# Kernel optimization log

Measured on AMD Instinct MI355X. Metric: run time of the kernel, lower is better.

## Reference

```python
import jax, jax.numpy as jnp
from jax import lax
import numpy as np

P = 9  # patch_size


def unfold9(img):
    # img: (C, H, W) -> (C, P*P, L) with L = (H//P)*(W//P), non-overlapping patches
    C, H, W = img.shape
    x = img.reshape(C, H // P, P, W // P, P)
    x = x.transpose(0, 2, 4, 1, 3).reshape(C, P * P, (H // P) * (W // P))
    return x


def fold9(blocks, H, W):
    # blocks: (C, P*P, L) -> (C, H, W), inverse of unfold9 (no overlaps)
    C = blocks.shape[0]
    x = blocks.reshape(C, P, P, H // P, W // P)
    return x.transpose(0, 3, 1, 4, 2).reshape(C, H, W)


def avgpool3d_k3s2p1(x):
    # AvgPool3d(kernel=3, stride=2, padding=1, count_include_pad=False) on (B,C,D,H,W)
    win = (1, 1, 3, 3, 3)
    strides = (1, 1, 2, 2, 2)
    pad = [(0, 0), (0, 0), (1, 1), (1, 1), (1, 1)]
    s = lax.reduce_window(x, 0.0, lax.add, win, strides, pad)
    cnt = lax.reduce_window(jnp.ones_like(x[:1, :1]), 0.0, lax.add, win, strides, pad)
    return s / cnt


def setup_inputs() -> dict:
    key = jax.random.key(0)
    k = jax.random.split(key, 7)
    in1, in2, out = 32, 64, 64
    x = jax.random.normal(k[0], (1, in1, 36, 72, 72), jnp.float32)
    y = jax.random.normal(k[1], (1, in2, 18, 36, 36), jnp.float32)
    z = jax.random.normal(k[2], (1, out, 36, 72, 72), jnp.float32)
    w_img = jax.random.normal(k[3], (out, in1), jnp.float32) * 0.05
    b_img = jax.random.normal(k[4], (out,), jnp.float32) * 0.01
    w_fea = jax.random.normal(k[5], (out, in2), jnp.float32) * 0.05
    b_fea = jax.random.normal(k[6], (out,), jnp.float32) * 0.01
    return {"x": x, "y": y, "z": z, "w_img": w_img, "b_img": b_img,
            "w_fea": w_fea, "b_fea": b_fea}


def reference(x, y, z, w_img, b_img, w_fea, b_fea):
    # 1x1x1 conv projections (pointwise channel mix)
    xq = jnp.einsum('bcdhw,oc->bodhw', x, w_img) + b_img[None, :, None, None, None]
    yk = jnp.einsum('bcdhw,oc->bodhw', y, w_fea) + b_fea[None, :, None, None, None]
    C = xq.shape[1]
    D1, HW1 = xq.shape[2], xq.shape[3] * xq.shape[4]
    D2, HW2 = yk.shape[2], yk.shape[3] * yk.shape[4]
    Ux = unfold9(xq.reshape(C, D1, HW1))          # (C, 81, L1)
    Uy = unfold9(yk.reshape(C, D2, HW2))          # (C, 81, L2)
    att = jnp.einsum('ckl,ckm->clm', Ux, Uy)      # (C, L1, L2) per-channel patch attn

    # --- Cross_head ---
    Dd, Hd, Wd = z.shape[2], z.shape[3], z.shape[4]
    dec = z.reshape(C, Dd, Hd * Wd)               # decoder_reshape
    xd = avgpool3d_k3s2p1(z)                      # (1, C, Dd', Hd', Wd')
    Dp, HWp = xd.shape[2], xd.shape[3] * xd.shape[4]
    Uxd = unfold9(xd.reshape(C, Dp, HWp))         # (C, 81, L2)
    # count_nonzero along L2 (non-differentiable, matches torch)
    nz = jnp.sum(att != 0, axis=-1).astype(att.dtype) + 1e-5  # (C, L1)
    corr_blocks = jnp.einsum('clm,ckm->ckl', att / nz[:, :, None], Uxd)  # (C, 81, L1)
    corr = fold9(corr_blocks, Dd, Hd * Wd)        # (C, Dd, Hd*Wd)
    act = jnp.where(corr > 0, corr, 0.2 * corr)   # LeakyReLU(0.2)
    out = act * dec + dec
    return out.reshape(z.shape)
```

## Files before the change

kernel.cpp:

```cpp
#include <hip/hip_runtime.h>
#include <hip/hip_bf16.h>

typedef __hip_bfloat16 bf16;
typedef float in_t;
typedef float out_t;
typedef __attribute__((ext_vector_type(8))) short short8;
typedef __attribute__((ext_vector_type(4))) float f32x4;

#define CH    64
#define CIN1  32
#define CIN2  64
#define S1    186624
#define W1    5184
#define S2    23328
#define W2    1296
#define BSTR  104
#define ASTR  104
#define OSTR  136
#define YSTR  68
#define HWSTR 76
#define INV_NZ (1.0f/(288.0f + 1e-5f))

#define NB_PL 2304
#define NB_PX 1458
#define NB_PY 365
#define NBT   (NB_PL + NB_PX + NB_PY)
#define NBR   (NBT - NB_PL)

static __device__ __forceinline__ unsigned short f2bu(float f) {
    bf16 h = __float2bfloat16(f);
    unsigned short u;
    __builtin_memcpy(&u, &h, 2);
    return u;
}

__global__ __launch_bounds__(256) void k_stage1(
    const in_t* __restrict__ x, const in_t* __restrict__ wi, const in_t* __restrict__ bi,
    bf16* __restrict__ xq,
    const in_t* __restrict__ y, const in_t* __restrict__ wf, const in_t* __restrict__ bf,
    unsigned short* __restrict__ yk,
    const in_t* __restrict__ z, unsigned short* __restrict__ xd)
{
    __shared__ __align__(16) char smem[17408];
    int t = threadIdx.x;
    long long i = blockIdx.x;

    long long pb = (i*NB_PL)/NBT;
    bool is_pool = ((i+1)*NB_PL)/NBT > pb;
    long long r  = i - pb;
    long long yb = (r*NB_PY)/NBR;
    bool is_py   = !is_pool && (((r+1)*NB_PY)/NBR > yb);

    if (is_pool) {
        int bid = (int)pb;
        float* dsum = reinterpret_cast<float*>(smem);
        int c  = bid / 36;
        int rr = bid - c*36;
        int od = rr >> 1, half = rr & 1;
        int hbase = half ? 35 : 0;
        int nrows = half ? 37 : 36;
        int oh0   = half ? 18 : 0;
        int dlo = od ? 2*od - 1 : 0;
        int nd  = od ? 3 : 2;
        const float* zb = z + ((size_t)c*36 + dlo)*W1;
        for (int ii = t; ii < nrows*18; ii += 256) {
            int rw = ii / 18, q = ii - (ii/18)*18;
            int off = (hbase + rw)*18 + q;
            const float4* p0 = reinterpret_cast<const float4*>(zb);
            float4 a = p0[off], b = p0[1296 + off];
            float4 s;
            if (nd == 3) {
                float4 e = p0[2592 + off];
                s = (float4){ a.x+b.x+e.x, a.y+b.y+e.y, a.z+b.z+e.z, a.w+b.w+e.w };
            } else {
                s = (float4){ a.x+b.x, a.y+b.y, a.z+b.z, a.w+b.w };
            }
            *reinterpret_cast<float4*>(&dsum[rw*HWSTR + q*4]) = s;
        }
        __syncthreads();
        float icd = (nd == 3) ? (1.f/3.f) : 0.5f;
        unsigned short* xdp = xd + (size_t)c*S2 + (size_t)od*W2 + oh0*36;
        for (int idx = t; idx < 648; idx += 256) {
            int ohl = idx / 36, ow = idx - (idx/36)*36;
            int oh = oh0 + ohl;
            int h0 = oh ? 2*oh-1 : 0, h1 = 2*oh+1;
            int w0 = ow ? 2*ow-1 : 0, w1 = 2*ow+1;
            float s = 0.f;
            for (int h = h0; h <= h1; ++h) {
                int lr = h - hbase;
                for (int w = w0; w <= w1; ++w)
                    s += dsum[lr*HWSTR + w];
            }
            float ich = (h1 - h0) == 1 ? 0.5f : (1.f/3.f);
            float icw = (w1 - w0) == 1 ? 0.5f : (1.f/3.f);
            xdp[idx] = f2bu(s * icd * ich * icw);
        }
    } else if (!is_py) {
        int gs0 = (int)(r - yb)*128;
        int l = t & 63, wv = t >> 6;
        int lcol = l & 15, loct = l >> 4;

        ushort4 rr4[2][4];
        #pragma unroll
        for (int mt = 0; mt < 2; ++mt) {
            int scol = gs0 + (wv*2 + mt)*16 + lcol;
            union { short8 v; unsigned short u[8]; } af;
            #pragma unroll
            for (int j = 0; j < 8; ++j)
                af.u[j] = f2bu(x[(size_t)(loct*8 + j)*S1 + scol]);
            #pragma unroll
            for (int og = 0; og < 4; ++og) {
                int o = og*16 + lcol;
                union { short8 v; unsigned short u[8]; } wfr;
                float4 a  = *reinterpret_cast<const float4*>(&wi[o*CIN1 + loct*8]);
                float4 bq = *reinterpret_cast<const float4*>(&wi[o*CIN1 + loct*8 + 4]);
                wfr.u[0]=f2bu(a.x);  wfr.u[1]=f2bu(a.y);
                wfr.u[2]=f2bu(a.z);  wfr.u[3]=f2bu(a.w);
                wfr.u[4]=f2bu(bq.x); wfr.u[5]=f2bu(bq.y);
                wfr.u[6]=f2bu(bq.z); wfr.u[7]=f2bu(bq.w);
                float bo = bi[o];
                f32x4 d = { bo, bo, bo, bo };
                d = __builtin_amdgcn_mfma_f32_16x16x32_bf16(af.v, wfr.v, d, 0, 0, 0);
                rr4[mt][og] = (ushort4){ f2bu(d[0]), f2bu(d[1]), f2bu(d[2]), f2bu(d[3]) };
            }
        }
        unsigned short* ot = reinterpret_cast<unsigned short*>(smem);
        #pragma unroll
        for (int mt = 0; mt < 2; ++mt)
            #pragma unroll
            for (int og = 0; og < 4; ++og)
                *reinterpret_cast<ushort4*>(
                    &ot[(og*16 + lcol)*OSTR + wv*32 + mt*16 + loct*4]) = rr4[mt][og];
        __syncthreads();
        #pragma unroll
        for (int j = 0; j < 4; ++j) {
            int row = wv*16 + j*4 + (l >> 4);
            int c8  = l & 15;
            uint4 v = *reinterpret_cast<const uint4*>(&ot[row*OSTR + c8*8]);
            *reinterpret_cast<uint4*>(
                (unsigned short*)xq + (size_t)row*S1 + gs0 + c8*8) = v;
        }
    } else {
        int pyb   = (int)yb;
        int sblk0 = pyb*64;
        int wv = t >> 6, l = t & 63;
        int lcol = l & 15, loct = l >> 4;
        int tile = pyb*4 + wv;
        unsigned short* ot = reinterpret_cast<unsigned short*>(smem);
        if (tile < 1458) {
            int s0 = tile*16;
            union { short8 v; unsigned short u[8]; } af[2];
            #pragma unroll
            for (int kk = 0; kk < 2; ++kk)
                #pragma unroll
                for (int j = 0; j < 8; ++j)
                    af[kk].u[j] = f2bu(y[(size_t)(kk*32 + loct*8 + j)*S2 + s0 + lcol]);
            #pragma unroll
            for (int og = 0; og < 4; ++og) {
                int o = og*16 + lcol;
                union { short8 v; unsigned short u[8]; } wfr[2];
                #pragma unroll
                for (int kk = 0; kk < 2; ++kk) {
                    float4 a  = *reinterpret_cast<const float4*>(&wf[o*CIN2 + kk*32 + loct*8]);
                    float4 bq = *reinterpret_cast<const float4*>(&wf[o*CIN2 + kk*32 + loct*8 + 4]);
                    wfr[kk].u[0]=f2bu(a.x);  wfr[kk].u[1]=f2bu(a.y);
                    wfr[kk].u[2]=f2bu(a.z);  wfr[kk].u[3]=f2bu(a.w);
                    wfr[kk].u[4]=f2bu(bq.x); wfr[kk].u[5]=f2bu(bq.y);
                    wfr[kk].u[6]=f2bu(bq.z); wfr[kk].u[7]=f2bu(bq.w);
                }
                float bo = bf[o];
                f32x4 d = { bo, bo, bo, bo };
                d = __builtin_amdgcn_mfma_f32_16x16x32_bf16(af[0].v, wfr[0].v, d, 0, 0, 0);
                d = __builtin_amdgcn_mfma_f32_16x16x32_bf16(af[1].v, wfr[1].v, d, 0, 0, 0);
                ushort4 r4 = { f2bu(d[0]), f2bu(d[1]), f2bu(d[2]), f2bu(d[3]) };
                *reinterpret_cast<ushort4*>(&ot[(og*16 + lcol)*YSTR + wv*16 + loct*4]) = r4;
            }
        }
        __syncthreads();
        #pragma unroll
        for (int j = 0; j < 4; ++j) {
            int row = wv*16 + j*4 + (l >> 4);
            int c4  = l & 15;
            int s   = sblk0 + c4*4;
            if (s < S2) {
                ushort4 v = *reinterpret_cast<const ushort4*>(&ot[row*YSTR + c4*4]);
                *reinterpret_cast<ushort4*>(&yk[(size_t)row*S2 + s]) = v;
            }
        }
    }
}

__global__ __launch_bounds__(256) void k_M(
    const unsigned short* __restrict__ xd, const unsigned short* __restrict__ yk,
    unsigned short* __restrict__ Mg)
{
    __shared__ __align__(16) unsigned short Al[96*ASTR];
    __shared__ __align__(16) unsigned short Bl[96*ASTR];
    int c = blockIdx.x;
    int t = threadIdx.x;
    int l = t & 63, wv = t >> 6;
    int lcol = l & 15, lhi = l >> 4;
    int wr = wv >> 1, wc = wv & 1;

    for (int idx = t; idx < 15*ASTR; idx += 256) {
        Al[81*ASTR + idx] = 0;
        Bl[81*ASTR + idx] = 0;
    }

    f32x4 acc[3][3];
    #pragma unroll
    for (int a = 0; a < 3; ++a)
        #pragma unroll
        for (int b = 0; b < 3; ++b)
            acc[a][b] = (f32x4){0.f,0.f,0.f,0.f};

    const unsigned short* xc = xd + (size_t)c*S2;
    const unsigned short* yc = yk + (size_t)c*S2;

    for (int q = 0; q < 3; ++q) {
        __syncthreads();
        for (int idx = t; idx < 1944; idx += 256) {
            int r18 = idx / 108, u4 = idx - r18*108;
            int srcoff = r18*W2 + q*432 + u4*4;
            ushort4 va = *reinterpret_cast<const ushort4*>(xc + srcoff);
            ushort4 vb = *reinterpret_cast<const ushort4*>(yc + srcoff);
            int ph2 = r18 / 9, i2 = r18 - ph2*9;
            unsigned short ua[4] = {va.x, va.y, va.z, va.w};
            unsigned short ub[4] = {vb.x, vb.y, vb.z, vb.w};
            #pragma unroll
            for (int j = 0; j < 4; ++j) {
                int cc  = u4*4 + j;
                int pw2 = cc / 9, j2 = cc - pw2*9;
                int row = i2*9 + j2;
                int mp  = pw2*2 + ph2;
                Al[row*ASTR + mp] = ua[j];
                Bl[row*ASTR + mp] = ub[j];
            }
        }
        __syncthreads();
        #pragma unroll
        for (int kk = 0; kk < 3; ++kk) {
            short8 afr[3], bfr[3];
            #pragma unroll
            for (int a = 0; a < 3; ++a)
                afr[a] = *reinterpret_cast<const short8*>(
                    &Al[(wr*48 + a*16 + lcol)*ASTR + kk*32 + lhi*8]);
            #pragma unroll
            for (int b = 0; b < 3; ++b)
                bfr[b] = *reinterpret_cast<const short8*>(
                    &Bl[(wc*48 + b*16 + lcol)*ASTR + kk*32 + lhi*8]);
            #pragma unroll
            for (int a = 0; a < 3; ++a)
                #pragma unroll
                for (int b = 0; b < 3; ++b)
                    acc[a][b] = __builtin_amdgcn_mfma_f32_16x16x32_bf16(
                        afr[a], bfr[b], acc[a][b], 0, 0, 0);
        }
    }
    unsigned short* Mc = Mg + (size_t)c*9216;
    #pragma unroll
    for (int a = 0; a < 3; ++a)
        #pragma unroll
        for (int b = 0; b < 3; ++b)
            #pragma unroll
            for (int rr = 0; rr < 4; ++rr) {
                int k1 = wr*48 + a*16 + lhi*4 + rr;
                int k2 = wc*48 + b*16 + lcol;
                Mc[k1*96 + k2] = f2bu(acc[a][b][rr]);
            }
}

__global__ __launch_bounds__(256, 4) void k_corr(
    const unsigned short* __restrict__ Mg, const bf16* __restrict__ xq,
    const in_t* __restrict__ z, out_t* __restrict__ out)
{
    __shared__ __align__(16) unsigned short Pl[192*BSTR];
    int bid = blockIdx.x;
    int c   = bid / 12;
    int rem = bid - c*12;
    int ph  = rem / 3;
    int ck  = rem - ph*3;
    int colbase = ck*1728;
    int t = threadIdx.x;

    for (int idx = t; idx < 192*15; idx += 256) {
        int r = idx/15;
        Pl[r*BSTR + 81 + (idx - r*15)] = 0;
    }
    const unsigned short* xqu =
        (const unsigned short*)(xq + (size_t)c*S1 + (size_t)(ph*9)*W1 + colbase);
    for (int idx = t; idx < 3888; idx += 256) {
        int i2 = idx / 432, v4 = idx - i2*432;
        ushort4 vv = *reinterpret_cast<const ushort4*>(xqu + (size_t)i2*W1 + v4*4);
        int col = v4*4;
        unsigned short uu[4] = {vv.x, vv.y, vv.z, vv.w};
        #pragma unroll
        for (int j = 0; j < 4; ++j) {
            int cc = col + j;
            int p = cc/9, j2 = cc - p*9;
            Pl[p*BSTR + i2*9 + j2] = uu[j];
        }
    }
    __syncthreads();

    int wv = t >> 6, l = t & 63;
    int lrow = l & 15, lhi = l >> 4;

    short8 bfr[3][3];
    #pragma unroll
    for (int ntl = 0; ntl < 3; ++ntl) {
        int n = (wv*3 + ntl)*16 + lrow;
        #pragma unroll
        for (int kk = 0; kk < 3; ++kk)
            bfr[ntl][kk] = *reinterpret_cast<const short8*>(&Pl[n*BSTR + kk*32 + lhi*8]);
    }

    f32x4 acc[6][3];
    #pragma unroll
    for (int mt = 0; mt < 6; ++mt)
        #pragma unroll
        for (int ntl = 0; ntl < 3; ++ntl)
            acc[mt][ntl] = (f32x4){0.f,0.f,0.f,0.f};

    const unsigned short* Mc = Mg + c*9216;
    #pragma unroll
    for (int mt = 0; mt < 6; ++mt) {
        short8 afr[3];
        #pragma unroll
        for (int kk = 0; kk < 3; ++kk)
            afr[kk] = *reinterpret_cast<const short8*>(Mc + (mt*16 + lrow)*96 + kk*32 + lhi*8);
        #pragma unroll
        for (int ntl = 0; ntl < 3; ++ntl) {
            f32x4 d = acc[mt][ntl];
            #pragma unroll
            for (int kk = 0; kk < 3; ++kk)
                d = __builtin_amdgcn_mfma_f32_16x16x32_bf16(afr[kk], bfr[ntl][kk], d, 0, 0, 0);
            acc[mt][ntl] = d;
        }
    }
    __syncthreads();

    float* stage = reinterpret_cast<float*>(Pl);
    #pragma unroll
    for (int pass = 0; pass < 2; ++pass) {
        if ((wv >> 1) == pass) {
            #pragma unroll
            for (int mt = 0; mt < 6; ++mt)
                #pragma unroll
                for (int ntl = 0; ntl < 3; ++ntl) {
                    int n = (wv*3 + ntl)*16 + lrow - pass*96;
                    #pragma unroll
                    for (int r = 0; r < 4; ++r) {
                        int m = mt*16 + lhi*4 + r;
                        if (m <= 80) {
                            int i = m/9, j = m - 9*i;
                            stage[i*864 + n*9 + j] = acc[mt][ntl][r];
                        }
                    }
                }
        }
        __syncthreads();
        for (int idx = t; idx < 1944; idx += 256) {
            int i = idx/216, c4 = idx - i*216;
            float4 sv = *reinterpret_cast<const float4*>(&stage[i*864 + c4*4]);
            int ga = c*S1 + (ph*9 + i)*W1 + colbase + pass*864 + c4*4;
            float4 dv = *reinterpret_cast<const float4*>(&z[ga]);
            float4 ov;
            float cr;
            cr = sv.x*INV_NZ; ov.x = dv.x + (cr > 0.f ? cr : 0.2f*cr)*dv.x;
            cr = sv.y*INV_NZ; ov.y = dv.y + (cr > 0.f ? cr : 0.2f*cr)*dv.y;
            cr = sv.z*INV_NZ; ov.z = dv.z + (cr > 0.f ? cr : 0.2f*cr)*dv.z;
            cr = sv.w*INV_NZ; ov.w = dv.w + (cr > 0.f ? cr : 0.2f*cr)*dv.w;
            *reinterpret_cast<float4*>(&out[ga]) = ov;
        }
        __syncthreads();
    }
}

extern "C" void kernel_launch(void* const* d_in, const int* in_sizes, int n_in,
                              void* d_out, int out_size, void* d_ws, size_t ws_size,
                              hipStream_t stream)
{
    (void)in_sizes; (void)n_in; (void)out_size; (void)ws_size;
    const in_t* x     = (const in_t*)d_in[0];
    const in_t* y     = (const in_t*)d_in[1];
    const in_t* z     = (const in_t*)d_in[2];
    const in_t* w_img = (const in_t*)d_in[3];
    const in_t* b_img = (const in_t*)d_in[4];
    const in_t* w_fea = (const in_t*)d_in[5];
    const in_t* b_fea = (const in_t*)d_in[6];
    out_t* out = (out_t*)d_out;

    char* ws = (char*)d_ws;
    bf16*           xq = (bf16*)          (ws + 0);
    unsigned short* yk = (unsigned short*)(ws + 23887872);
    unsigned short* xd = (unsigned short*)(ws + 26873856);
    unsigned short* Mg = (unsigned short*)(ws + 29859840);

    hipLaunchKernelGGL(k_stage1, dim3(NBT), dim3(256), 0, stream,
                       x, w_img, b_img, xq, y, w_fea, b_fea, yk, z, xd);
    hipLaunchKernelGGL(k_M,      dim3(64),  dim3(256), 0, stream, xd, yk, Mg);
    hipLaunchKernelGGL(k_corr,   dim3(768), dim3(256), 0, stream, Mg, xq, z, out);
}
```

Measured before the change: 66.26 us.

## Fuse per-channel M computation into k_corr and drop the separate k_M launch

The k_M kernel is folded into k_corr. Each k_corr block now recomputes the 96x96 per-channel M matrix from xd and yk in shared memory and reads it from LDS, instead of reading it from a global buffer written by a separate 64-block launch. This removes one kernel launch, the global round trip for M, and a stage that ran on only 64 blocks. In exchange, M is recomputed 12 times per channel, which adds xd/yk loads and MFMA work to every block. The larger shared-memory footprint also lowers the occupancy bound from 4 to 2 blocks per CU.

```diff
diff --git a/kernel.cpp b/kernel.cpp
--- a/kernel.cpp
+++ b/kernel.cpp
@@ -15,7 +15,6 @@
 #define S2    23328
 #define W2    1296
 #define BSTR  104
-#define ASTR  104
 #define OSTR  136
 #define YSTR  68
 #define HWSTR 76
@@ -190,33 +189,39 @@
     }
 }
 
-__global__ __launch_bounds__(256) void k_M(
+__global__ __launch_bounds__(256, 2) void k_corr(
     const unsigned short* __restrict__ xd, const unsigned short* __restrict__ yk,
-    unsigned short* __restrict__ Mg)
+    const bf16* __restrict__ xq, const in_t* __restrict__ z, out_t* __restrict__ out)
 {
-    __shared__ __align__(16) unsigned short Al[96*ASTR];
-    __shared__ __align__(16) unsigned short Bl[96*ASTR];
-    int c = blockIdx.x;
+    __shared__ __align__(16) char smem[59904];
+    unsigned short* Al = reinterpret_cast<unsigned short*>(smem);
+    unsigned short* Bl = reinterpret_cast<unsigned short*>(smem) + 96*BSTR;
+    unsigned short* Ml = reinterpret_cast<unsigned short*>(smem) + 2*96*BSTR;
+    unsigned short* Pl = reinterpret_cast<unsigned short*>(smem);
+    int bid = blockIdx.x;
+    int c   = bid / 12;
+    int rem = bid - c*12;
+    int ph  = rem / 3;
+    int ck  = rem - ph*3;
+    int colbase = ck*1728;
     int t = threadIdx.x;
-    int l = t & 63, wv = t >> 6;
+    int wv = t >> 6, l = t & 63;
     int lcol = l & 15, lhi = l >> 4;
+
     int wr = wv >> 1, wc = wv & 1;
-
-    for (int idx = t; idx < 15*ASTR; idx += 256) {
-        Al[81*ASTR + idx] = 0;
-        Bl[81*ASTR + idx] = 0;
-    }
-
-    f32x4 acc[3][3];
+    for (int idx = t; idx < 15*BSTR; idx += 256) {
+        Al[81*BSTR + idx] = 0;
+        Bl[81*BSTR + idx] = 0;
+    }
+    f32x4 macc[3][3];
     #pragma unroll
     for (int a = 0; a < 3; ++a)
         #pragma unroll
         for (int b = 0; b < 3; ++b)
-            acc[a][b] = (f32x4){0.f,0.f,0.f,0.f};
+            macc[a][b] = (f32x4){0.f,0.f,0.f,0.f};
 
     const unsigned short* xc = xd + (size_t)c*S2;
     const unsigned short* yc = yk + (size_t)c*S2;
-
     for (int q = 0; q < 3; ++q) {
         __syncthreads();
         for (int idx = t; idx < 1944; idx += 256) {
@@ -233,8 +238,8 @@
                 int pw2 = cc / 9, j2 = cc - pw2*9;
                 int row = i2*9 + j2;
                 int mp  = pw2*2 + ph2;
-                Al[row*ASTR + mp] = ua[j];
-                Bl[row*ASTR + mp] = ub[j];
+                Al[row*BSTR + mp] = ua[j];
+                Bl[row*BSTR + mp] = ub[j];
             }
         }
         __syncthreads();
@@ -244,20 +249,19 @@
             #pragma unroll
             for (int a = 0; a < 3; ++a)
                 afr[a] = *reinterpret_cast<const short8*>(
-                    &Al[(wr*48 + a*16 + lcol)*ASTR + kk*32 + lhi*8]);
+                    &Al[(wr*48 + a*16 + lcol)*BSTR + kk*32 + lhi*8]);
             #pragma unroll
             for (int b = 0; b < 3; ++b)
                 bfr[b] = *reinterpret_cast<const short8*>(
-                    &Bl[(wc*48 + b*16 + lcol)*ASTR + kk*32 + lhi*8]);
+                    &Bl[(wc*48 + b*16 + lcol)*BSTR + kk*32 + lhi*8]);
             #pragma unroll
             for (int a = 0; a < 3; ++a)
                 #pragma unroll
                 for (int b = 0; b < 3; ++b)
-                    acc[a][b] = __builtin_amdgcn_mfma_f32_16x16x32_bf16(
-                        afr[a], bfr[b], acc[a][b], 0, 0, 0);
-        }
-    }
-    unsigned short* Mc = Mg + (size_t)c*9216;
+                    macc[a][b] = __builtin_amdgcn_mfma_f32_16x16x32_bf16(
+                        afr[a], bfr[b], macc[a][b], 0, 0, 0);
+        }
+    }
     #pragma unroll
     for (int a = 0; a < 3; ++a)
         #pragma unroll
@@ -266,22 +270,9 @@
             for (int rr = 0; rr < 4; ++rr) {
                 int k1 = wr*48 + a*16 + lhi*4 + rr;
                 int k2 = wc*48 + b*16 + lcol;
-                Mc[k1*96 + k2] = f2bu(acc[a][b][rr]);
-            }
-}
-
-__global__ __launch_bounds__(256, 4) void k_corr(
-    const unsigned short* __restrict__ Mg, const bf16* __restrict__ xq,
-    const in_t* __restrict__ z, out_t* __restrict__ out)
-{
-    __shared__ __align__(16) unsigned short Pl[192*BSTR];
-    int bid = blockIdx.x;
-    int c   = bid / 12;
-    int rem = bid - c*12;
-    int ph  = rem / 3;
-    int ck  = rem - ph*3;
-    int colbase = ck*1728;
-    int t = threadIdx.x;
+                Ml[k1*BSTR + k2] = f2bu(macc[a][b][rr]);
+            }
+    __syncthreads();
 
     for (int idx = t; idx < 192*15; idx += 256) {
         int r = idx/15;
@@ -303,8 +294,7 @@
     }
     __syncthreads();
 
-    int wv = t >> 6, l = t & 63;
-    int lrow = l & 15, lhi = l >> 4;
+    int lrow = l & 15;
 
     short8 bfr[3][3];
     #pragma unroll
@@ -322,13 +312,13 @@
         for (int ntl = 0; ntl < 3; ++ntl)
             acc[mt][ntl] = (f32x4){0.f,0.f,0.f,0.f};
 
-    const unsigned short* Mc = Mg + c*9216;
     #pragma unroll
     for (int mt = 0; mt < 6; ++mt) {
         short8 afr[3];
         #pragma unroll
         for (int kk = 0; kk < 3; ++kk)
-            afr[kk] = *reinterpret_cast<const short8*>(Mc + (mt*16 + lrow)*96 + kk*32 + lhi*8);
+            afr[kk] = *reinterpret_cast<const short8*>(
+                &Ml[(mt*16 + lrow)*BSTR + kk*32 + lhi*8]);
         #pragma unroll
         for (int ntl = 0; ntl < 3; ++ntl) {
             f32x4 d = acc[mt][ntl];
@@ -395,10 +385,8 @@
     bf16*           xq = (bf16*)          (ws + 0);
     unsigned short* yk = (unsigned short*)(ws + 23887872);
     unsigned short* xd = (unsigned short*)(ws + 26873856);
-    unsigned short* Mg = (unsigned short*)(ws + 29859840);
 
     hipLaunchKernelGGL(k_stage1, dim3(NBT), dim3(256), 0, stream,
                        x, w_img, b_img, xq, y, w_fea, b_fea, yk, z, xd);
-    hipLaunchKernelGGL(k_M,      dim3(64),  dim3(256), 0, stream, xd, yk, Mg);
-    hipLaunchKernelGGL(k_corr,   dim3(768), dim3(256), 0, stream, Mg, xq, z, out);
+    hipLaunchKernelGGL(k_corr,   dim3(768), dim3(256), 0, stream, xd, yk, xq, z, out);
 }
```

After: 83.36 us. 1.26x slower.
